# Kernel tuning notes

Hardware: AMD Instinct MI355X
Metric: run time of the kernel (lower is better)

## Reference

```python
import jax, jax.numpy as jnp
import numpy as np

EPSILON = 1e-13
LN_EPS = 1e-5
DIRECTIONS = 2
HID = 512


def setup_inputs() -> dict:
    key = jax.random.key(0)
    k1, k2, k3, k4 = jax.random.split(key, 4)
    B, N, D = 16, 1024, HID
    adj = jax.random.randint(k1, (B, N, N), 0, 3, dtype=jnp.int32)  # labels 0..2
    hid = jax.random.normal(k2, (B, N, D), dtype=jnp.float32)
    W = jax.random.normal(k3, (DIRECTIONS * D, D), dtype=jnp.float32) * (1.0 / np.sqrt(DIRECTIONS * D))
    b = jnp.zeros((D,), dtype=jnp.float32)
    gamma = jnp.ones((D,), dtype=jnp.float32)
    beta = jnp.zeros((D,), dtype=jnp.float32)
    return {"adj": adj, "hid": hid, "W": W, "b": b, "gamma": gamma, "beta": beta}


def _layer_norm(x, gamma, beta):
    mu = jnp.mean(x, axis=-1, keepdims=True)
    var = jnp.mean(jnp.square(x - mu), axis=-1, keepdims=True)
    return (x - mu) * jax.lax.rsqrt(var + LN_EPS) * gamma + beta


def reference(adj, hid, W, b, gamma, beta):
    residual = hid
    direct_list = []
    for j in range(DIRECTIONS):  # fixed small structural loop
        mask = (adj == (j + 1)).astype(hid.dtype)            # [B,N,N]
        weight = mask / (jnp.sum(mask, axis=-1, keepdims=True) + EPSILON)
        direct_list.append(jnp.einsum('bnm,bmd->bnd', weight, hid))
    out = jnp.concatenate(direct_list, axis=-1)              # [B,N,directions*D]
    out = out @ W + b                                        # [B,N,D]
    out = jax.nn.relu(out)
    out = out + residual
    return _layer_norm(out, gamma, beta)
```

## Files before the change

### kernel.cpp

```cpp
#include <hip/hip_runtime.h>

#define NB 16
#define NN 1024
#define ND 512

typedef __attribute__((ext_vector_type(8))) short short8;
typedef __attribute__((ext_vector_type(4))) float f32x4;

typedef const __attribute__((address_space(1))) void* gptr1;
typedef __attribute__((address_space(3))) void* lptr3;

#define VMCNT0() asm volatile("s_waitcnt vmcnt(0)" ::: "memory")
#define VMCNT4() asm volatile("s_waitcnt vmcnt(4)" ::: "memory")
#define VMCNT8() asm volatile("s_waitcnt vmcnt(8)" ::: "memory")
#define LGKM0()  asm volatile("s_waitcnt lgkmcnt(0)" ::: "memory")
#define BAR()    __builtin_amdgcn_s_barrier()

union U8 { uint4 u; short8 s; };

static __device__ __forceinline__ unsigned f2bf(float f) {
  union { float f; unsigned u; } v; v.f = f;
  unsigned r = v.u + 0x7FFFu + ((v.u >> 16) & 1u);
  return r >> 16;
}
static __device__ __forceinline__ float bf2f(unsigned short h) {
  union { unsigned u; float f; } v; v.u = ((unsigned)h) << 16;
  return v.f;
}

__global__ void k_wtcat(const float* __restrict__ W, unsigned short* __restrict__ WTcat) {
  __shared__ float t[64][65];
  int dir = blockIdx.z;
  int r0 = blockIdx.x * 64;
  int c0 = blockIdx.y * 64;
  int tid = threadIdx.x;
#pragma unroll
  for (int i = 0; i < 4; ++i) {
    int f = i * 256 + tid;
    int r = f >> 4, cq = f & 15;
    float4 v = *(const float4*)(W + (size_t)(dir * 512 + r0 + r) * ND + c0 + cq * 4);
    t[r][cq * 4 + 0] = v.x; t[r][cq * 4 + 1] = v.y;
    t[r][cq * 4 + 2] = v.z; t[r][cq * 4 + 3] = v.w;
  }
  __syncthreads();
#pragma unroll
  for (int i = 0; i < 8; ++i) {
    int f = i * 256 + tid;
    int oc = f >> 5;
    int on = (f & 31) * 2;
    unsigned lo = f2bf(t[on][oc]), hi = f2bf(t[on + 1][oc]);
    *(unsigned*)(WTcat + (size_t)(dir * 512 + c0 + oc) * ND + r0 + on) = lo | (hi << 16);
  }
}

__global__ void k_pack(const int* __restrict__ adj, unsigned* __restrict__ packed,
                       float* __restrict__ invc) {
  int wid = threadIdx.x >> 6, lane = threadIdx.x & 63;
  int wrow0 = (blockIdx.x * 4 + wid) * 4;
  int pl = (lane & ~3) | ((lane & 1) << 1) | ((lane >> 1) & 1);
#pragma unroll
  for (int r = 0; r < 4; ++r) {
    int row = wrow0 + r;
    const int* p = adj + (size_t)row * NN + lane * 16;
    unsigned u = 0;
#pragma unroll
    for (int i = 0; i < 4; ++i) {
      int4 v = *(const int4*)(p + i * 4);
      u |= ((unsigned)v.x << (8 * i)) | ((unsigned)v.y << (8 * i + 2))
         | ((unsigned)v.z << (8 * i + 4)) | ((unsigned)v.w << (8 * i + 6));
    }
    packed[(size_t)row * 64 + pl] = u;
    unsigned c1 = __popc(u & 0x55555555u);
    unsigned c2 = __popc(u & 0xAAAAAAAAu);
    unsigned pr = c1 | (c2 << 16);
#pragma unroll
    for (int o = 32; o; o >>= 1) pr += __shfl_xor(pr, o);
    if (lane == 0) {
      invc[row * 2 + 0] = 1.0f / ((float)(pr & 0xFFFFu) + 1e-13f);
      invc[row * 2 + 1] = 1.0f / ((float)(pr >> 16) + 1e-13f);
    }
  }
}

__global__ __launch_bounds__(256, 2) void k_pre(
    const float* __restrict__ hid, const unsigned short* __restrict__ WTcat,
    unsigned short* __restrict__ Ptcat) {
  __shared__ __align__(16) char smem[49152];
  char* Bh = smem + 32768;

  int phys = blockIdx.x;
  int logical = (phys & 7) * 128 + (phys >> 3);
  int b = logical >> 6;
  int rem = logical & 63;
  int rt = rem >> 3, mt = rem & 7;
  int r0 = rt * 128, m0 = mt * 128;

  int tid = threadIdx.x, lane = tid & 63, wid = tid >> 6;
  int wr = wid >> 1, wc = wid & 1;
  int l15 = lane & 15, lq = lane >> 4;
  int srow = lane >> 3;
  int ssl = (lane & 7) ^ srow;

  const float* hb = hid + (size_t)b * NN * ND;

  f32x4 acc[4][4];
  f32x4 zero = {0.f, 0.f, 0.f, 0.f};
#pragma unroll
  for (int i = 0; i < 4; ++i)
#pragma unroll
    for (int j = 0; j < 4; ++j) acc[i][j] = zero;

  float4 fc[8], fn[8];
#pragma unroll
  for (int it = 0; it < 8; ++it) {
    int f = it * 256 + tid;
    fc[it] = *(const float4*)(hb + (size_t)(m0 + (f >> 4)) * ND + (f & 15) * 4);
  }
#pragma unroll
  for (int i = 0; i < 4; ++i) {
    int q = wid * 4 + i;
    int r = q * 8 + srow;
    __builtin_amdgcn_global_load_lds((gptr1)(WTcat + (size_t)(r0 + r) * ND + ssl * 8),
                                     (lptr3)(smem + q * 1024), 16, 0, 0);
  }

#pragma unroll 1
  for (int kt = 0; kt < 8; ++kt) {
    int k0 = kt * 64;
#pragma unroll
    for (int it = 0; it < 8; ++it) {
      int f = it * 256 + tid;
      int row = f >> 4, c4 = f & 15;
      float4 v = fc[it];
      unsigned lo = f2bf(v.x) | (f2bf(v.y) << 16);
      unsigned hi = f2bf(v.z) | (f2bf(v.w) << 16);
      int addr = row * 128 + (((c4 >> 1) ^ (row & 7)) * 16) + (c4 & 1) * 8;
      *(uint2*)(Bh + addr) = make_uint2(lo, hi);
    }
    if (kt < 7) {
#pragma unroll
      for (int it = 0; it < 8; ++it) {
        int f = it * 256 + tid;
        fn[it] = *(const float4*)(hb + (size_t)(m0 + (f >> 4)) * ND + k0 + 64 + (f & 15) * 4);
      }
      VMCNT8();
    } else {
      VMCNT0();
    }
    LGKM0();
    BAR();
    if (kt < 7) {
      char* ab = smem + (((kt + 1) & 1) << 14);
#pragma unroll
      for (int i = 0; i < 4; ++i) {
        int q = wid * 4 + i;
        int r = q * 8 + srow;
        __builtin_amdgcn_global_load_lds((gptr1)(WTcat + (size_t)(r0 + r) * ND + k0 + 64 + ssl * 8),
                                         (lptr3)(ab + q * 1024), 16, 0, 0);
      }
    }
    const char* ac = smem + ((kt & 1) << 14);
    __builtin_amdgcn_s_setprio(1);
#pragma unroll
    for (int ks = 0; ks < 2; ++ks) {
      short8 a[4], bf[4];
#pragma unroll
      for (int mi = 0; mi < 4; ++mi) {
        int row = wr * 64 + mi * 16 + l15;
        int slot = (ks * 4 + lq) ^ (l15 & 7);
        a[mi] = *(const short8*)(ac + row * 128 + slot * 16);
      }
#pragma unroll
      for (int nj = 0; nj < 4; ++nj) {
        int col = wc * 64 + nj * 16 + l15;
        int slot = (ks * 4 + lq) ^ (l15 & 7);
        bf[nj] = *(const short8*)(Bh + col * 128 + slot * 16);
      }
#pragma unroll
      for (int mi = 0; mi < 4; ++mi)
#pragma unroll
        for (int nj = 0; nj < 4; ++nj)
          acc[mi][nj] = __builtin_amdgcn_mfma_f32_16x16x32_bf16(a[mi], bf[nj], acc[mi][nj], 0, 0, 0);
    }
    __builtin_amdgcn_s_setprio(0);
    BAR();
    if (kt < 7) {
#pragma unroll
      for (int it = 0; it < 8; ++it) fc[it] = fn[it];
    }
    __builtin_amdgcn_sched_barrier(0);
  }
  unsigned short* Pb = Ptcat + (size_t)b * NN * NN;
#pragma unroll
  for (int mi = 0; mi < 4; ++mi) {
#pragma unroll
    for (int rr = 0; rr < 4; ++rr) {
      int r = r0 + wr * 64 + mi * 16 + lq * 4 + rr;
#pragma unroll
      for (int nj = 0; nj < 4; ++nj) {
        int m = m0 + wc * 64 + nj * 16 + l15;
        Pb[(size_t)r * NN + m] = (unsigned short)f2bf(acc[mi][nj][rr]);
      }
    }
  }
}

__global__ __launch_bounds__(256, 2) void k_main(
    const unsigned* __restrict__ packed, const unsigned short* __restrict__ Ptcat,
    const float* __restrict__ invc, const float* __restrict__ bias,
    const float* __restrict__ hid, unsigned short* __restrict__ preS) {
  __shared__ __align__(16) char smB[32768];

  int phys = blockIdx.x;
  int logical = (phys & 7) * 64 + (phys >> 3);
  int b = logical >> 5;
  int rem = logical & 31;
  int mt = rem >> 2, dt = rem & 3;
  int n0 = mt * 128, d0 = dt * 128;

  int tid = threadIdx.x, lane = tid & 63, wid = tid >> 6;
  int wr = wid >> 1, wc = wid & 1;
  int l15 = lane & 15, lq = lane >> 4;
  int h2 = lq >> 1;
  int srow = lane >> 3;
  int ssl = (lane & 7) ^ srow;
  size_t bN = (size_t)b * NN;

  const unsigned* cbase[4];
#pragma unroll
  for (int mi = 0; mi < 4; ++mi)
    cbase[mi] = packed + (bN + n0 + wr * 64 + mi * 16 + l15) * 64 + 2 * h2;

  const unsigned short* Ptb = Ptcat + bN * NN;

  const char* base0 = smB + (wc * 64 + l15) * 128 + ((lq ^ (l15 & 7)) * 16);
  const char* base1 = smB + (wc * 64 + l15) * 128 + (((4 + lq) ^ (l15 & 7)) * 16);

  f32x4 accA[4][4], accB[4][4];
  f32x4 zero = {0.f, 0.f, 0.f, 0.f};
#pragma unroll
  for (int i = 0; i < 4; ++i)
#pragma unroll
    for (int j = 0; j < 4; ++j) { accA[i][j] = zero; accB[i][j] = zero; }

  uint2 cA[4], cB[4];
#pragma unroll
  for (int mi = 0; mi < 4; ++mi) cA[mi] = *(const uint2*)(cbase[mi]);
#pragma unroll
  for (int i = 0; i < 4; ++i) {
    int q = wid * 4 + i;
    __builtin_amdgcn_global_load_lds((gptr1)(Ptb + (size_t)(d0 + q * 8 + srow) * NN + ssl * 8),
                                     (lptr3)(smB + q * 1024), 16, 0, 0);
  }
#pragma unroll
  for (int mi = 0; mi < 4; ++mi) cB[mi] = *(const uint2*)(cbase[mi] + 4);

  unsigned shb = (unsigned)((lq & 1) * 16);

#define KT_BODY(KT_, CSET, ACC)                                               \
  {                                                                           \
    int kt = (KT_);                                                           \
    if (kt == 31) { VMCNT0(); } else { VMCNT4(); }                            \
    BAR();                                                                    \
    if (kt < 31) {                                                            \
      int t = kt + 1; int dirn = t >> 4; int k0n = (t & 15) * 64;             \
      _Pragma("unroll")                                                       \
      for (int i = 0; i < 4; ++i) {                                           \
        int q = wid * 4 + i;                                                  \
        __builtin_amdgcn_global_load_lds(                                     \
          (gptr1)(Ptb + (size_t)(dirn * 512 + d0 + q * 8 + srow) * NN + k0n + ssl * 8), \
          (lptr3)(smB + ((~kt & 1) << 14) + q * 1024), 16, 0, 0);             \
      }                                                                       \
    }                                                                         \
    const char* bb0 = base0 + ((kt & 1) << 14);                               \
    const char* bb1 = base1 + ((kt & 1) << 14);                               \
    short8 bf0[4], bf1[4];                                                    \
    _Pragma("unroll")                                                         \
    for (int nj = 0; nj < 4; ++nj) {                                          \
      bf0[nj] = *(const short8*)(bb0 + nj * 2048);                            \
      bf1[nj] = *(const short8*)(bb1 + nj * 2048);                            \
    }                                                                         \
    U8 a0[4], a1[4];                                                          \
    _Pragma("unroll")                                                         \
    for (int mi = 0; mi < 4; ++mi) {                                          \
      unsigned cd0 = CSET[mi].x >> shb;                                       \
      unsigned cd1 = CSET[mi].y >> shb;                                       \
      _Pragma("unroll")                                                       \
      for (int j = 0; j < 4; ++j) {                                           \
        unsigned t5 = (cd0 >> (4 * j)) & 5u;                                  \
        a0[mi].u[j] = ((t5 | (t5 << 14)) & 0x00010001u) * 0x3F80u;            \
        unsigned s5 = (cd1 >> (4 * j)) & 5u;                                  \
        a1[mi].u[j] = ((s5 | (s5 << 14)) & 0x00010001u) * 0x3F80u;            \
      }                                                                       \
    }                                                                         \
    __builtin_amdgcn_s_setprio(1);                                            \
    _Pragma("unroll")                                                         \
    for (int nj = 0; nj < 4; ++nj)                                            \
      _Pragma("unroll")                                                       \
      for (int mi = 0; mi < 4; ++mi)                                          \
        ACC[mi][nj] = __builtin_amdgcn_mfma_f32_16x16x32_bf16(a0[mi].s, bf0[nj], ACC[mi][nj], 0, 0, 0); \
    _Pragma("unroll")                                                         \
    for (int nj = 0; nj < 4; ++nj)                                            \
      _Pragma("unroll")                                                       \
      for (int mi = 0; mi < 4; ++mi)                                          \
        ACC[mi][nj] = __builtin_amdgcn_mfma_f32_16x16x32_bf16(a1[mi].s, bf1[nj], ACC[mi][nj], 0, 0, 0); \
    __builtin_amdgcn_s_setprio(0);                                            \
    if (kt < 30) {                                                            \
      int g2 = (kt + 2) & 15;                                                 \
      _Pragma("unroll")                                                       \
      for (int mi = 0; mi < 4; ++mi)                                          \
        CSET[mi] = *(const uint2*)(cbase[mi] + g2 * 4);                       \
    }                                                                         \
  }

#pragma unroll 1
  for (int kk = 0; kk < 8; ++kk) {
    KT_BODY(kk * 2,     cA, accA)
    KT_BODY(kk * 2 + 1, cB, accA)
  }
  shb = (unsigned)((lq & 1) * 16 + 1);
#pragma unroll 1
  for (int kk = 8; kk < 16; ++kk) {
    KT_BODY(kk * 2,     cA, accB)
    KT_BODY(kk * 2 + 1, cB, accB)
  }
#undef KT_BODY

#pragma unroll
  for (int mi = 0; mi < 4; ++mi) {
#pragma unroll
    for (int rr = 0; rr < 4; ++rr) {
      int n = n0 + wr * 64 + mi * 16 + lq * 4 + rr;
      float i1 = invc[(bN + n) * 2 + 0];
      float i2 = invc[(bN + n) * 2 + 1];
      const float* hrow = hid + (bN + n) * ND;
      unsigned short* prow = preS + (bN + n) * ND;
#pragma unroll
      for (int nj = 0; nj < 4; ++nj) {
        int d = d0 + wc * 64 + nj * 16 + l15;
        float v = accA[mi][nj][rr] * i1 + accB[mi][nj][rr] * i2 + bias[d];
        v = fmaxf(v, 0.f);
        v += hrow[d];
        prow[d] = (unsigned short)f2bf(v);
      }
    }
  }
}

__global__ void k_ln(const unsigned short* __restrict__ preS, float* __restrict__ out,
                     const float* __restrict__ gamma, const float* __restrict__ beta) {
  int row = blockIdx.x * 4 + (threadIdx.x >> 6);
  int lane = threadIdx.x & 63;
  short8 raw = *(const short8*)(preS + (size_t)row * ND + lane * 8);
  float x[8];
#pragma unroll
  for (int i = 0; i < 8; ++i) x[i] = bf2f((unsigned short)raw[i]);
  float s = 0.f;
#pragma unroll
  for (int i = 0; i < 8; ++i) s += x[i];
#pragma unroll
  for (int o = 32; o; o >>= 1) s += __shfl_xor(s, o);
  float mu = s * (1.0f / 512.0f);
  float v = 0.f;
#pragma unroll
  for (int i = 0; i < 8; ++i) { float d = x[i] - mu; v += d * d; }
#pragma unroll
  for (int o = 32; o; o >>= 1) v += __shfl_xor(v, o);
  float rs = rsqrtf(v * (1.0f / 512.0f) + 1e-5f);
  float4 g0 = *(const float4*)(gamma + lane * 8);
  float4 g1 = *(const float4*)(gamma + lane * 8 + 4);
  float4 b0 = *(const float4*)(beta + lane * 8);
  float4 b1 = *(const float4*)(beta + lane * 8 + 4);
  float4 y0, y1;
  y0.x = (x[0] - mu) * rs * g0.x + b0.x; y0.y = (x[1] - mu) * rs * g0.y + b0.y;
  y0.z = (x[2] - mu) * rs * g0.z + b0.z; y0.w = (x[3] - mu) * rs * g0.w + b0.w;
  y1.x = (x[4] - mu) * rs * g1.x + b1.x; y1.y = (x[5] - mu) * rs * g1.y + b1.y;
  y1.z = (x[6] - mu) * rs * g1.z + b1.z; y1.w = (x[7] - mu) * rs * g1.w + b1.w;
  float* p = out + (size_t)row * ND + lane * 8;
  *(float4*)p = y0;
  *(float4*)(p + 4) = y1;
}

extern "C" void kernel_launch(void* const* d_in, const int* in_sizes, int n_in,
                              void* d_out, int out_size, void* d_ws, size_t ws_size,
                              hipStream_t stream) {
  (void)in_sizes; (void)n_in; (void)out_size; (void)ws_size;
  const int*   adj   = (const int*)d_in[0];
  const float* hid   = (const float*)d_in[1];
  const float* W     = (const float*)d_in[2];
  const float* bias  = (const float*)d_in[3];
  const float* gamma = (const float*)d_in[4];
  const float* beta  = (const float*)d_in[5];
  float* out = (float*)d_out;

  char* ws = (char*)d_ws;
  unsigned short* WTcat  = (unsigned short*)ws;
  unsigned short* preS   = (unsigned short*)ws;
  unsigned short* Ptcat  = (unsigned short*)(ws + 16777216);
  unsigned*       packed = (unsigned*)(ws + 50331648);
  float*          invc   = (float*)(ws + 54525952);

  k_wtcat<<<dim3(8, 8, 2), 256, 0, stream>>>(W, WTcat);
  k_pack <<<1024, 256, 0, stream>>>(adj, packed, invc);
  k_pre  <<<1024, 256, 0, stream>>>(hid, WTcat, Ptcat);
  k_main <<<512, 256, 0, stream>>>(packed, Ptcat, invc, bias, hid, preS);
  k_ln   <<<4096, 256, 0, stream>>>(preS, out, gamma, beta);
}
```

Measured before the change: 112.9 us.

## Double-buffer B tile in k_pre and widen k_main K-step to 128

k_pre now double-buffers the converted hid tile in LDS and writes the next tile after the MFMA block, which removes one barrier per iteration and lets the conversion overlap compute. k_main doubles its LDS tile to cover 128 K-columns per step, halving iteration count and barriers. It loads wider uint4 adjacency words, with the packing permutation in k_pack changed to match. LDS use grows to 64KB per block, which may limit occupancy to fewer blocks per CU.

```diff
diff --git a/kernel.cpp b/kernel.cpp
--- a/kernel.cpp
+++ b/kernel.cpp
@@ -15,6 +15,7 @@
 #define VMCNT8() asm volatile("s_waitcnt vmcnt(8)" ::: "memory")
 #define LGKM0()  asm volatile("s_waitcnt lgkmcnt(0)" ::: "memory")
 #define BAR()    __builtin_amdgcn_s_barrier()
+#define SCHED0() __builtin_amdgcn_sched_barrier(0)
 
 union U8 { uint4 u; short8 s; };
 
@@ -57,7 +58,7 @@
                        float* __restrict__ invc) {
   int wid = threadIdx.x >> 6, lane = threadIdx.x & 63;
   int wrow0 = (blockIdx.x * 4 + wid) * 4;
-  int pl = (lane & ~3) | ((lane & 1) << 1) | ((lane >> 1) & 1);
+  int pl = (lane & ~7) | ((lane & 1) << 2) | ((lane >> 1) & 3);
 #pragma unroll
   for (int r = 0; r < 4; ++r) {
     int row = wrow0 + r;
@@ -85,8 +86,7 @@
 __global__ __launch_bounds__(256, 2) void k_pre(
     const float* __restrict__ hid, const unsigned short* __restrict__ WTcat,
     unsigned short* __restrict__ Ptcat) {
-  __shared__ __align__(16) char smem[49152];
-  char* Bh = smem + 32768;
+  __shared__ __align__(16) char smem[65536];
 
   int phys = blockIdx.x;
   int logical = (phys & 7) * 128 + (phys >> 3);
@@ -110,86 +110,105 @@
 #pragma unroll
     for (int j = 0; j < 4; ++j) acc[i][j] = zero;
 
-  float4 fc[8], fn[8];
+  float4 fA[8], fB[8];
 #pragma unroll
   for (int it = 0; it < 8; ++it) {
     int f = it * 256 + tid;
-    fc[it] = *(const float4*)(hb + (size_t)(m0 + (f >> 4)) * ND + (f & 15) * 4);
+    fA[it] = *(const float4*)(hb + (size_t)(m0 + (f >> 4)) * ND + (f & 15) * 4);
   }
 #pragma unroll
   for (int i = 0; i < 4; ++i) {
     int q = wid * 4 + i;
-    int r = q * 8 + srow;
-    __builtin_amdgcn_global_load_lds((gptr1)(WTcat + (size_t)(r0 + r) * ND + ssl * 8),
+    __builtin_amdgcn_global_load_lds((gptr1)(WTcat + (size_t)(r0 + q * 8 + srow) * ND + ssl * 8),
                                      (lptr3)(smem + q * 1024), 16, 0, 0);
   }
+#pragma unroll
+  for (int it = 0; it < 8; ++it) {
+    int f = it * 256 + tid;
+    int row = f >> 4, c4 = f & 15;
+    float4 v = fA[it];
+    unsigned lo = f2bf(v.x) | (f2bf(v.y) << 16);
+    unsigned hi = f2bf(v.z) | (f2bf(v.w) << 16);
+    int addr = row * 128 + (((c4 >> 1) ^ (row & 7)) * 16) + (c4 & 1) * 8;
+    *(uint2*)(smem + 32768 + addr) = make_uint2(lo, hi);
+  }
+#pragma unroll
+  for (int it = 0; it < 8; ++it) {
+    int f = it * 256 + tid;
+    fB[it] = *(const float4*)(hb + (size_t)(m0 + (f >> 4)) * ND + 64 + (f & 15) * 4);
+  }
+  LGKM0(); VMCNT8();
+
+#define PRE_BODY(KT_, FCUR, FNXT)                                             \
+  {                                                                           \
+    int kt = (KT_);                                                           \
+    BAR();                                                                    \
+    if (kt < 7) {                                                             \
+      char* ab = smem + ((~kt & 1) << 14);                                    \
+      _Pragma("unroll")                                                       \
+      for (int i = 0; i < 4; ++i) {                                           \
+        int q = wid * 4 + i;                                                  \
+        __builtin_amdgcn_global_load_lds(                                     \
+          (gptr1)(WTcat + (size_t)(r0 + q * 8 + srow) * ND + (kt + 1) * 64 + ssl * 8), \
+          (lptr3)(ab + q * 1024), 16, 0, 0);                                  \
+      }                                                                       \
+      SCHED0();                                                               \
+    }                                                                         \
+    const char* ac = smem + ((kt & 1) << 14);                                 \
+    const char* bc = smem + 32768 + ((kt & 1) << 14);                         \
+    __builtin_amdgcn_s_setprio(1);                                            \
+    _Pragma("unroll")                                                         \
+    for (int ks = 0; ks < 2; ++ks) {                                          \
+      short8 a[4], bf[4];                                                     \
+      _Pragma("unroll")                                                       \
+      for (int mi = 0; mi < 4; ++mi) {                                        \
+        int slot = (ks * 4 + lq) ^ (l15 & 7);                                 \
+        a[mi] = *(const short8*)(ac + (wr * 64 + mi * 16 + l15) * 128 + slot * 16); \
+      }                                                                       \
+      _Pragma("unroll")                                                       \
+      for (int nj = 0; nj < 4; ++nj) {                                        \
+        int slot = (ks * 4 + lq) ^ (l15 & 7);                                 \
+        bf[nj] = *(const short8*)(bc + (wc * 64 + nj * 16 + l15) * 128 + slot * 16); \
+      }                                                                       \
+      _Pragma("unroll")                                                       \
+      for (int mi = 0; mi < 4; ++mi)                                          \
+        _Pragma("unroll")                                                     \
+        for (int nj = 0; nj < 4; ++nj)                                        \
+          acc[mi][nj] = __builtin_amdgcn_mfma_f32_16x16x32_bf16(a[mi], bf[nj], acc[mi][nj], 0, 0, 0); \
+    }                                                                         \
+    __builtin_amdgcn_s_setprio(0);                                            \
+    if (kt < 7) {                                                             \
+      char* bn = smem + 32768 + ((~kt & 1) << 14);                            \
+      _Pragma("unroll")                                                       \
+      for (int it = 0; it < 8; ++it) {                                        \
+        int f = it * 256 + tid;                                               \
+        int row = f >> 4, c4 = f & 15;                                        \
+        float4 v = FCUR[it];                                                  \
+        unsigned lo = f2bf(v.x) | (f2bf(v.y) << 16);                          \
+        unsigned hi = f2bf(v.z) | (f2bf(v.w) << 16);                          \
+        int addr = row * 128 + (((c4 >> 1) ^ (row & 7)) * 16) + (c4 & 1) * 8; \
+        *(uint2*)(bn + addr) = make_uint2(lo, hi);                            \
+      }                                                                       \
+    }                                                                         \
+    if (kt < 6) {                                                             \
+      _Pragma("unroll")                                                       \
+      for (int it = 0; it < 8; ++it) {                                        \
+        int f = it * 256 + tid;                                               \
+        FNXT[it] = *(const float4*)(hb + (size_t)(m0 + (f >> 4)) * ND + (kt + 2) * 64 + (f & 15) * 4); \
+      }                                                                       \
+      LGKM0(); VMCNT8();                                                      \
+    } else if (kt < 7) {                                                      \
+      LGKM0(); VMCNT0();                                                      \
+    }                                                                         \
+  }
 
 #pragma unroll 1
-  for (int kt = 0; kt < 8; ++kt) {
-    int k0 = kt * 64;
-#pragma unroll
-    for (int it = 0; it < 8; ++it) {
-      int f = it * 256 + tid;
-      int row = f >> 4, c4 = f & 15;
-      float4 v = fc[it];
-      unsigned lo = f2bf(v.x) | (f2bf(v.y) << 16);
-      unsigned hi = f2bf(v.z) | (f2bf(v.w) << 16);
-      int addr = row * 128 + (((c4 >> 1) ^ (row & 7)) * 16) + (c4 & 1) * 8;
-      *(uint2*)(Bh + addr) = make_uint2(lo, hi);
-    }
-    if (kt < 7) {
-#pragma unroll
-      for (int it = 0; it < 8; ++it) {
-        int f = it * 256 + tid;
-        fn[it] = *(const float4*)(hb + (size_t)(m0 + (f >> 4)) * ND + k0 + 64 + (f & 15) * 4);
-      }
-      VMCNT8();
-    } else {
-      VMCNT0();
-    }
-    LGKM0();
-    BAR();
-    if (kt < 7) {
-      char* ab = smem + (((kt + 1) & 1) << 14);
-#pragma unroll
-      for (int i = 0; i < 4; ++i) {
-        int q = wid * 4 + i;
-        int r = q * 8 + srow;
-        __builtin_amdgcn_global_load_lds((gptr1)(WTcat + (size_t)(r0 + r) * ND + k0 + 64 + ssl * 8),
-                                         (lptr3)(ab + q * 1024), 16, 0, 0);
-      }
-    }
-    const char* ac = smem + ((kt & 1) << 14);
-    __builtin_amdgcn_s_setprio(1);
-#pragma unroll
-    for (int ks = 0; ks < 2; ++ks) {
-      short8 a[4], bf[4];
-#pragma unroll
-      for (int mi = 0; mi < 4; ++mi) {
-        int row = wr * 64 + mi * 16 + l15;
-        int slot = (ks * 4 + lq) ^ (l15 & 7);
-        a[mi] = *(const short8*)(ac + row * 128 + slot * 16);
-      }
-#pragma unroll
-      for (int nj = 0; nj < 4; ++nj) {
-        int col = wc * 64 + nj * 16 + l15;
-        int slot = (ks * 4 + lq) ^ (l15 & 7);
-        bf[nj] = *(const short8*)(Bh + col * 128 + slot * 16);
-      }
-#pragma unroll
-      for (int mi = 0; mi < 4; ++mi)
-#pragma unroll
-        for (int nj = 0; nj < 4; ++nj)
-          acc[mi][nj] = __builtin_amdgcn_mfma_f32_16x16x32_bf16(a[mi], bf[nj], acc[mi][nj], 0, 0, 0);
-    }
-    __builtin_amdgcn_s_setprio(0);
-    BAR();
-    if (kt < 7) {
-#pragma unroll
-      for (int it = 0; it < 8; ++it) fc[it] = fn[it];
-    }
-    __builtin_amdgcn_sched_barrier(0);
-  }
+  for (int kk = 0; kk < 4; ++kk) {
+    PRE_BODY(kk * 2,     fB, fA)
+    PRE_BODY(kk * 2 + 1, fA, fB)
+  }
+#undef PRE_BODY
+
   unsigned short* Pb = Ptcat + (size_t)b * NN * NN;
 #pragma unroll
   for (int mi = 0; mi < 4; ++mi) {
@@ -209,7 +228,7 @@
     const unsigned* __restrict__ packed, const unsigned short* __restrict__ Ptcat,
     const float* __restrict__ invc, const float* __restrict__ bias,
     const float* __restrict__ hid, unsigned short* __restrict__ preS) {
-  __shared__ __align__(16) char smB[32768];
+  __shared__ __align__(16) char smB[65536];
 
   int phys = blockIdx.x;
   int logical = (phys & 7) * 64 + (phys >> 3);
@@ -221,20 +240,17 @@
   int tid = threadIdx.x, lane = tid & 63, wid = tid >> 6;
   int wr = wid >> 1, wc = wid & 1;
   int l15 = lane & 15, lq = lane >> 4;
-  int h2 = lq >> 1;
+  int h2 = (lq >> 1) & 1;
   int srow = lane >> 3;
   int ssl = (lane & 7) ^ srow;
   size_t bN = (size_t)b * NN;
 
-  const unsigned* cbase[4];
-#pragma unroll
-  for (int mi = 0; mi < 4; ++mi)
-    cbase[mi] = packed + (bN + n0 + wr * 64 + mi * 16 + l15) * 64 + 2 * h2;
-
+  const unsigned* cpb = packed + (bN + n0 + wr * 64 + l15) * 64 + h2 * 4;
   const unsigned short* Ptb = Ptcat + bN * NN;
 
-  const char* base0 = smB + (wc * 64 + l15) * 128 + ((lq ^ (l15 & 7)) * 16);
-  const char* base1 = smB + (wc * 64 + l15) * 128 + (((4 + lq) ^ (l15 & 7)) * 16);
+  int rowbase = (d0 + wid * 32 + srow) * NN + ssl * 8;
+  int fo0 = (wc * 64 + l15) * 128 + ((lq ^ (l15 & 7)) * 16);
+  int fo1 = (wc * 64 + l15) * 128 + (((4 + lq) ^ (l15 & 7)) * 16);
 
   f32x4 accA[4][4], accB[4][4];
   f32x4 zero = {0.f, 0.f, 0.f, 0.f};
@@ -243,84 +259,82 @@
 #pragma unroll
     for (int j = 0; j < 4; ++j) { accA[i][j] = zero; accB[i][j] = zero; }
 
-  uint2 cA[4], cB[4];
-#pragma unroll
-  for (int mi = 0; mi < 4; ++mi) cA[mi] = *(const uint2*)(cbase[mi]);
+  uint4 cA[4], cB[4];
+#pragma unroll
+  for (int mi = 0; mi < 4; ++mi) cA[mi] = *(const uint4*)(cpb + mi * 1024);
 #pragma unroll
   for (int i = 0; i < 4; ++i) {
-    int q = wid * 4 + i;
-    __builtin_amdgcn_global_load_lds((gptr1)(Ptb + (size_t)(d0 + q * 8 + srow) * NN + ssl * 8),
-                                     (lptr3)(smB + q * 1024), 16, 0, 0);
-  }
-#pragma unroll
-  for (int mi = 0; mi < 4; ++mi) cB[mi] = *(const uint2*)(cbase[mi] + 4);
+    __builtin_amdgcn_global_load_lds((gptr1)(Ptb + rowbase + i * 8192),
+                                     (lptr3)(smB + (wid * 4 + i) * 1024), 16, 0, 0);
+    __builtin_amdgcn_global_load_lds((gptr1)(Ptb + rowbase + i * 8192 + 64),
+                                     (lptr3)(smB + 16384 + (wid * 4 + i) * 1024), 16, 0, 0);
+  }
+  SCHED0();
+#pragma unroll
+  for (int mi = 0; mi < 4; ++mi) cB[mi] = *(const uint4*)(cpb + mi * 1024 + 8);
 
   unsigned shb = (unsigned)((lq & 1) * 16);
 
 #define KT_BODY(KT_, CSET, ACC)                                               \
   {                                                                           \
     int kt = (KT_);                                                           \
-    if (kt == 31) { VMCNT0(); } else { VMCNT4(); }                            \
+    if (kt == 15) { VMCNT0(); } else { VMCNT4(); }                            \
     BAR();                                                                    \
-    if (kt < 31) {                                                            \
-      int t = kt + 1; int dirn = t >> 4; int k0n = (t & 15) * 64;             \
+    if (kt < 15) {                                                            \
+      int t = kt + 1;                                                         \
+      int koff = ((t & 7) << 7) + ((t >> 3) << 19);                           \
+      char* db = smB + ((~kt & 1) << 15);                                     \
       _Pragma("unroll")                                                       \
       for (int i = 0; i < 4; ++i) {                                           \
-        int q = wid * 4 + i;                                                  \
-        __builtin_amdgcn_global_load_lds(                                     \
-          (gptr1)(Ptb + (size_t)(dirn * 512 + d0 + q * 8 + srow) * NN + k0n + ssl * 8), \
-          (lptr3)(smB + ((~kt & 1) << 14) + q * 1024), 16, 0, 0);             \
-      }                                                                       \
-    }                                                                         \
-    const char* bb0 = base0 + ((kt & 1) << 14);                               \
-    const char* bb1 = base1 + ((kt & 1) << 14);                               \
-    short8 bf0[4], bf1[4];                                                    \
+        __builtin_amdgcn_global_load_lds((gptr1)(Ptb + rowbase + i * 8192 + koff), \
+            (lptr3)(db + (wid * 4 + i) * 1024), 16, 0, 0);                    \
+        __builtin_amdgcn_global_load_lds((gptr1)(Ptb + rowbase + i * 8192 + koff + 64), \
+            (lptr3)(db + 16384 + (wid * 4 + i) * 1024), 16, 0, 0);            \
+      }                                                                       \
+      SCHED0();                                                               \
+    }                                                                         \
+    const char* bb = smB + ((kt & 1) << 15);                                  \
     _Pragma("unroll")                                                         \
-    for (int nj = 0; nj < 4; ++nj) {                                          \
-      bf0[nj] = *(const short8*)(bb0 + nj * 2048);                            \
-      bf1[nj] = *(const short8*)(bb1 + nj * 2048);                            \
-    }                                                                         \
-    U8 a0[4], a1[4];                                                          \
-    _Pragma("unroll")                                                         \
-    for (int mi = 0; mi < 4; ++mi) {                                          \
-      unsigned cd0 = CSET[mi].x >> shb;                                       \
-      unsigned cd1 = CSET[mi].y >> shb;                                       \
-      _Pragma("unroll")                                                       \
-      for (int j = 0; j < 4; ++j) {                                           \
-        unsigned t5 = (cd0 >> (4 * j)) & 5u;                                  \
-        a0[mi].u[j] = ((t5 | (t5 << 14)) & 0x00010001u) * 0x3F80u;            \
-        unsigned s5 = (cd1 >> (4 * j)) & 5u;                                  \
-        a1[mi].u[j] = ((s5 | (s5 << 14)) & 0x00010001u) * 0x3F80u;            \
-      }                                                                       \
-    }                                                                         \
-    __builtin_amdgcn_s_setprio(1);                                            \
-    _Pragma("unroll")                                                         \
-    for (int nj = 0; nj < 4; ++nj)                                            \
+    for (int ks = 0; ks < 4; ++ks) {                                          \
+      const char* bp = bb + ((ks >> 1) << 14) + ((ks & 1) ? fo1 : fo0);       \
+      short8 bf[4];                                                           \
+      _Pragma("unroll")                                                       \
+      for (int nj = 0; nj < 4; ++nj) bf[nj] = *(const short8*)(bp + nj * 2048); \
+      U8 a[4];                                                                \
+      _Pragma("unroll")                                                       \
+      for (int mi = 0; mi < 4; ++mi) {                                        \
+        unsigned wd = (ks == 0) ? CSET[mi].x : (ks == 1) ? CSET[mi].y         \
+                     : (ks == 2) ? CSET[mi].z : CSET[mi].w;                   \
+        unsigned cd = wd >> shb;                                              \
+        _Pragma("unroll")                                                     \
+        for (int j = 0; j < 4; ++j) {                                         \
+          unsigned t5 = (cd >> (4 * j)) & 5u;                                 \
+          a[mi].u[j] = ((t5 | (t5 << 14)) & 0x00010001u) * 0x3F80u;           \
+        }                                                                     \
+      }                                                                       \
+      __builtin_amdgcn_s_setprio(1);                                          \
+      _Pragma("unroll")                                                       \
+      for (int nj = 0; nj < 4; ++nj)                                          \
+        _Pragma("unroll")                                                     \
+        for (int mi = 0; mi < 4; ++mi)                                        \
+          ACC[mi][nj] = __builtin_amdgcn_mfma_f32_16x16x32_bf16(a[mi].s, bf[nj], ACC[mi][nj], 0, 0, 0); \
+      __builtin_amdgcn_s_setprio(0);                                          \
+    }                                                                         \
+    if (kt < 14) {                                                            \
       _Pragma("unroll")                                                       \
       for (int mi = 0; mi < 4; ++mi)                                          \
-        ACC[mi][nj] = __builtin_amdgcn_mfma_f32_16x16x32_bf16(a0[mi].s, bf0[nj], ACC[mi][nj], 0, 0, 0); \
-    _Pragma("unroll")                                                         \
-    for (int nj = 0; nj < 4; ++nj)                                            \
-      _Pragma("unroll")                                                       \
-      for (int mi = 0; mi < 4; ++mi)                                          \
-        ACC[mi][nj] = __builtin_amdgcn_mfma_f32_16x16x32_bf16(a1[mi].s, bf1[nj], ACC[mi][nj], 0, 0, 0); \
-    __builtin_amdgcn_s_setprio(0);                                            \
-    if (kt < 30) {                                                            \
-      int g2 = (kt + 2) & 15;                                                 \
-      _Pragma("unroll")                                                       \
-      for (int mi = 0; mi < 4; ++mi)                                          \
-        CSET[mi] = *(const uint2*)(cbase[mi] + g2 * 4);                       \
+        CSET[mi] = *(const uint4*)(cpb + mi * 1024 + ((kt + 2) & 7) * 8);     \
     }                                                                         \
   }
 
 #pragma unroll 1
-  for (int kk = 0; kk < 8; ++kk) {
+  for (int kk = 0; kk < 4; ++kk) {
     KT_BODY(kk * 2,     cA, accA)
     KT_BODY(kk * 2 + 1, cB, accA)
   }
   shb = (unsigned)((lq & 1) * 16 + 1);
 #pragma unroll 1
-  for (int kk = 8; kk < 16; ++kk) {
+  for (int kk = 4; kk < 8; ++kk) {
     KT_BODY(kk * 2,     cA, accB)
     KT_BODY(kk * 2 + 1, cB, accB)
   }
```

Result: slower. 129.4 us (+14.6%).
